# Optimization experiments

Hardware: AMD Instinct MI355X
Metric: run time of the kernel (lower is better)

Reference implementation:

```python
import jax, jax.numpy as jnp
import numpy as np
from jax import lax

SCORE_T = 0.05
NMS_T = 0.5
MAXDET = 300


def batch_iou(b1, b2):
    # b1: [K,4], b2: [K,4] -> [K,K]
    lt = jnp.maximum(b1[:, None, :2], b2[None, :, :2])
    rb = jnp.minimum(b1[:, None, 2:], b2[None, :, 2:])
    inter = jnp.clip(rb - lt, 0.0, None).prod(-1)
    a1 = (b1[:, 2:] - b1[:, :2]).prod(-1)
    a2 = (b2[:, 2:] - b2[:, :2]).prod(-1)
    union = a1[:, None] + a2[None, :] - inter
    return inter / jnp.clip(union, 1e-7, None)


def nms_class(boxes, cls_scores):
    # boxes: [N,4], cls_scores: [N]. Mirrors: score>thresh filter, top-k MAXDET
    # candidates, greedy NMS in descending score order.
    s = jnp.where(cls_scores > SCORE_T, cls_scores, -jnp.inf)
    top_s, idx = lax.top_k(s, MAXDET)          # sorted desc, [K]
    b = jnp.take(boxes, idx, axis=0)            # [K,4]
    v = jnp.isfinite(top_s)                     # passed score threshold
    iou = batch_iou(b, b)                       # [K,K]

    def body(kept, i):
        # keep i iff valid and no already-kept box has IoU >= NMS_T with it
        suppressed = jnp.any(jnp.where(kept, iou[i], 0.0) >= NMS_T)
        return kept.at[i].set(v[i] & ~suppressed), None

    kept, _ = lax.scan(body, jnp.zeros(MAXDET, dtype=bool), jnp.arange(MAXDET))
    return top_s, idx, kept


def per_image(boxes, cls):
    # boxes: [N,4], cls: [N,C]
    C = cls.shape[1]
    top_s, idx, kept = jax.vmap(nms_class, in_axes=(None, 1))(boxes, cls)  # [C,K]
    scores_flat = jnp.where(kept, top_s, -jnp.inf).reshape(-1)  # [C*K]
    idx_flat = idx.reshape(-1)
    labels_flat = jnp.repeat(jnp.arange(C), MAXDET)
    fs, fi = lax.top_k(scores_flat, MAXDET)     # global top-k across classes
    valid = jnp.isfinite(fs)
    box_idx = idx_flat[fi]
    out_boxes = jnp.where(valid[:, None], jnp.take(boxes, box_idx, axis=0), -1.0)
    out_scores = jnp.where(valid, fs, -1.0)
    out_labels = jnp.where(valid, labels_flat[fi], -1).astype(jnp.int32)
    return out_boxes, out_scores, out_labels


def setup_inputs() -> dict:
    key = jax.random.key(0)
    k1, k2, k3 = jax.random.split(key, 3)
    B, N, C = 8, 100000, 80
    centers = jax.random.uniform(k1, (B, N, 2), dtype=jnp.float32) * 1024.0
    wh = jax.random.uniform(k2, (B, N, 2), dtype=jnp.float32) * 96.0 + 4.0
    boxes = jnp.concatenate([centers - wh / 2, centers + wh / 2], axis=-1)
    classification = jax.random.uniform(k3, (B, N, C), dtype=jnp.float32)
    return {"boxes": boxes, "classification": classification}


def reference(boxes, classification):
    # Returns (Boxes [B,MAXDET,4], Scores [B,MAXDET], Labels [B,MAXDET] int32),
    # padded with -1 where fewer than MAXDET detections survive.
    return jax.vmap(per_image)(boxes, classification)
```

## Files before the change

kernel.cpp:

```cpp
#include <hip/hip_runtime.h>

#define BIMG 8
#define NBOX 100000
#define NCLS 80
#define KDET 300
#define CAP  2048
#define CAPC 12
#define TPUSH 0.9921875f
#define SCORE_T 0.05f
#define NELEM 8000000
#define NQ    2000000

typedef unsigned long long u64;
typedef unsigned u32;

#define OFF_PUSHCNT 0u
#define OFF_IMGDONE 2560u
#define ZERO_BYTES  2592u
#define OFF_BUF     4096u
#define OFF_KCNT    (4096u + 10485760u)
#define OFF_KSC     (OFF_KCNT + 2560u)
#define OFF_KIDX    (OFF_KSC + 768000u)

static __device__ __forceinline__ u64 mk_key(float sc, u32 n) {
  return ((u64)__float_as_uint(sc) << 32) | (u32)(~n);
}

static __device__ __forceinline__ void radix_step(const u32* hist, int nbins,
                                                  int width, u32* sk, u64* spfx,
                                                  u32* stot) {
  if (threadIdx.x < 64) {
    const int lane = threadIdx.x;
    const int chunk = nbins >> 6;
    u32 psum = 0;
    for (int i = 0; i < chunk; ++i) psum += hist[lane * chunk + i];
    u32 suf = psum;
#pragma unroll
    for (int off = 1; off < 64; off <<= 1) {
      u32 o = __shfl_down(suf, off);
      if (lane + off < 64) suf += o;
    }
    if (lane == 0) *stot = suf;
    u32 k = *sk;
    u64 bal = __ballot(suf >= k);
    if (bal != 0ull) {
      int L = 63 - __clzll((long long)bal);
      if (lane == L) {
        u32 krem = k - (suf - psum);
        int bi = (L + 1) * chunk - 1;
        u32 acc = 0;
        for (;;) {
          acc += hist[bi];
          if (acc >= krem || bi == L * chunk) break;
          --bi;
        }
        *spfx = (*spfx << width) | (u32)bi;
        *sk = krem - (acc - hist[bi]);
      }
    }
  }
}

__constant__ int RSH[6] = {53, 42, 31, 20, 9, 0};
__constant__ int RWD[6] = {11, 11, 11, 11, 11, 9};

static __device__ __forceinline__ void bitonic512(u64* tk, int t) {
  u64 a = tk[t];
#pragma unroll
  for (int k2 = 2; k2 <= 64; k2 <<= 1) {
#pragma unroll
    for (int j = k2 >> 1; j > 0; j >>= 1) {
      u64 c2 = __shfl_xor(a, j);
      bool takeMax = (((t & k2) == 0) == ((t & j) == 0));
      u64 mx = (a > c2) ? a : c2;
      u64 mn = (a > c2) ? c2 : a;
      a = takeMax ? mx : mn;
    }
  }
#pragma unroll
  for (int k2 = 128; k2 <= 512; k2 <<= 1) {
    for (int j = k2 >> 1; j >= 64; j >>= 1) {
      tk[t] = a;
      __syncthreads();
      u64 c2 = tk[t ^ j];
      bool takeMax = (((t & k2) == 0) == ((t & j) == 0));
      u64 mx = (a > c2) ? a : c2;
      u64 mn = (a > c2) ? c2 : a;
      a = takeMax ? mx : mn;
      __syncthreads();
    }
#pragma unroll
    for (int j = 32; j > 0; j >>= 1) {
      u64 c2 = __shfl_xor(a, j);
      bool takeMax = (((t & k2) == 0) == ((t & j) == 0));
      u64 mx = (a > c2) ? a : c2;
      u64 mn = (a > c2) ? c2 : a;
      a = takeMax ? mx : mn;
    }
  }
  tk[t] = a;
  __syncthreads();
}

static __device__ __forceinline__ void pushone(int c, float sc, u32 n, int b,
                                               u32* lcnt, u64* stage,
                                               u32* pushcnt, u64* buf) {
  u64 key = mk_key(sc, n);
  u32 slot = atomicAdd(&lcnt[c], 1u);
  if (slot < CAPC) {
    stage[c * CAPC + slot] = key;
  } else {
    u32 g = atomicAdd(&pushcnt[b * NCLS + c], 1u);
    if (g < CAP) buf[(size_t)(b * NCLS + c) * CAP + g] = key;
  }
}

__global__ __launch_bounds__(256) void histK(const float* __restrict__ cls,
                                             u32* __restrict__ pushcnt,
                                             u64* __restrict__ buf) {
  __shared__ u32 lcnt[NCLS];
  __shared__ u32 sbase[NCLS];
  __shared__ u64 stage[NCLS * CAPC];

  const int t = threadIdx.x;
  const int b = blockIdx.y;
  for (int i = t; i < NCLS; i += 256) lcnt[i] = 0;
  __syncthreads();

  const float4* base4 = (const float4*)(cls + (size_t)b * NELEM);
  const int start = blockIdx.x * 8192;

#define PROCQ(u) do { \
    float mx = fmaxf(fmaxf(v##u.x, v##u.y), fmaxf(v##u.z, v##u.w)); \
    if (mx >= TPUSH) { \
      const int e0 = q##u * 4; \
      const int c0 = e0 % NCLS; \
      const u32 n = (u32)(e0 / NCLS); \
      if (v##u.x >= TPUSH) pushone(c0 + 0, v##u.x, n, b, lcnt, stage, pushcnt, buf); \
      if (v##u.y >= TPUSH) pushone(c0 + 1, v##u.y, n, b, lcnt, stage, pushcnt, buf); \
      if (v##u.z >= TPUSH) pushone(c0 + 2, v##u.z, n, b, lcnt, stage, pushcnt, buf); \
      if (v##u.w >= TPUSH) pushone(c0 + 3, v##u.w, n, b, lcnt, stage, pushcnt, buf); \
    } } while (0)

  if (start + 8192 <= NQ) {
    for (int it = 0; it < 4; ++it) {
      const int qb = start + it * 2048 + t;
#define LOADF(u) const int q##u = qb + (u) * 256; const float4 v##u = base4[q##u]
      LOADF(0); LOADF(1); LOADF(2); LOADF(3);
      LOADF(4); LOADF(5); LOADF(6); LOADF(7);
#undef LOADF
      PROCQ(0); PROCQ(1); PROCQ(2); PROCQ(3);
      PROCQ(4); PROCQ(5); PROCQ(6); PROCQ(7);
    }
  } else {
    for (int it = 0; it < 4; ++it) {
      const int qb = start + it * 2048 + t;
#define LOADC(u) const int q##u = qb + (u) * 256; \
  const float4 v##u = (q##u < NQ) ? base4[q##u] : make_float4(0.f, 0.f, 0.f, 0.f)
      LOADC(0); LOADC(1); LOADC(2); LOADC(3);
      LOADC(4); LOADC(5); LOADC(6); LOADC(7);
#undef LOADC
      PROCQ(0); PROCQ(1); PROCQ(2); PROCQ(3);
      PROCQ(4); PROCQ(5); PROCQ(6); PROCQ(7);
    }
  }
#undef PROCQ
  __syncthreads();

  if (t < NCLS) {
    u32 cnt = min(lcnt[t], (u32)CAPC);
    sbase[t] = cnt ? atomicAdd(&pushcnt[b * NCLS + t], cnt) : 0u;
  }
  __syncthreads();
  for (int idx = t; idx < NCLS * CAPC; idx += 256) {
    const int c = idx / CAPC;
    const int k = idx - c * CAPC;
    if ((u32)k < min(lcnt[c], (u32)CAPC)) {
      u32 s = sbase[c] + (u32)k;
      if (s < CAP) buf[(size_t)(b * NCLS + c) * CAP + s] = stage[idx];
    }
  }
}

__global__ __launch_bounds__(512) void nmsK(const float* __restrict__ boxes,
                                            const float* __restrict__ cls,
                                            const u32* __restrict__ pushcnt,
                                            u64* __restrict__ buf,
                                            u32* __restrict__ keptCnt,
                                            float* __restrict__ keptScore,
                                            u32* __restrict__ keptIdx,
                                            u32* __restrict__ imgDone,
                                            float* __restrict__ out) {
  __shared__ float bx[KDET][4];
  __shared__ float scl[KDET];
  __shared__ u32 nn_[KDET];
  __shared__ u64 msk[KDET][5];
  __shared__ u64 tk[512];
  __shared__ u64 keptw[5];
  __shared__ u64 spfx;
  __shared__ u64 sand, sor;
  __shared__ u32 sk, stot, stcnt, smtot, smerge;
  __shared__ int msc[NCLS];
  __shared__ u32 sfpfx, sfk, sfab, sfeq, sfmode, sfbcnt;

  const int t = threadIdx.x;
  const int bc = blockIdx.x;
  const int b = bc / NCLS;
  u64* bufp = buf + (size_t)bc * CAP;
  u32* hist = (u32*)&msk[0][0];

  if (t == 0) { spfx = 0ull; sk = KDET; stcnt = 0u; sfmode = 0u; sfbcnt = 0u; }

  u32 realcnt = pushcnt[bc];
  const bool dofb = !(realcnt >= (u32)KDET && realcnt <= (u32)CAP);
  if (dofb) {
    const int c = bc % NCLS;
    const float* col = cls + (size_t)b * NELEM + c;
    for (int r = 0; r < 3; ++r) {
      const int shift = (r == 0) ? 21 : (r == 1) ? 10 : 0;
      const int nbins = (r == 2) ? 1024 : 2048;
      for (int i = t; i < nbins; i += 512) hist[i] = 0;
      __syncthreads();
      for (int n = t; n < NBOX; n += 512) {
        float sc = col[(size_t)n * NCLS];
        if (sc > SCORE_T) {
          u32 u = __float_as_uint(sc);
          bool ok = (r == 0) || (r == 1 ? ((u >> 21) == (sfpfx >> 21))
                                        : ((u >> 10) == (sfpfx >> 10)));
          if (ok) atomicAdd(&hist[(u >> shift) & (u32)(nbins - 1)], 1u);
        }
      }
      __syncthreads();
      if (t == 0) {
        if (r == 0) {
          u32 s = 0;
          for (int i = 0; i < nbins; ++i) s += hist[i];
          if (s < KDET) sfmode = 1u;
        }
        if (sfmode == 0u) {
          u32 kk2 = (r == 0) ? (u32)KDET : sfk;
          u32 acc = 0;
          int bi = nbins - 1;
          for (; bi >= 0; --bi) {
            if (acc + hist[bi] >= kk2) break;
            acc += hist[bi];
          }
          sfk = kk2 - acc;
          sfpfx = ((r == 0) ? 0u : sfpfx) | ((u32)bi << shift);
          if (r == 2) { sfeq = hist[bi]; sfab = KDET - sfk; }
        }
      }
      __syncthreads();
      if (sfmode == 1u) break;
    }

    if (sfmode == 1u) {
      for (int n = t; n < NBOX; n += 512) {
        float sc = col[(size_t)n * NCLS];
        if (sc > SCORE_T) {
          u32 g = atomicAdd(&sfbcnt, 1u);
          if (g < CAP) bufp[g] = mk_key(sc, (u32)n);
        }
      }
    } else {
      const u32 ustar = sfpfx;
      const u32 m = sfab, e = sfeq;
      if (m + e <= CAP) {
        for (int n = t; n < NBOX; n += 512) {
          float sc = col[(size_t)n * NCLS];
          if (sc > SCORE_T && __float_as_uint(sc) >= ustar) {
            u32 g = atomicAdd(&sfbcnt, 1u);
            if (g < CAP) bufp[g] = mk_key(sc, (u32)n);
          }
        }
      } else {
        for (int n = t; n < NBOX; n += 512) {
          float sc = col[(size_t)n * NCLS];
          if (sc > SCORE_T && __float_as_uint(sc) > ustar) {
            u32 g = atomicAdd(&sfbcnt, 1u);
            if (g < CAP) bufp[g] = mk_key(sc, (u32)n);
          }
        }
        __syncthreads();
        if (t == 0) {
          u32 room = CAP - m, got = 0;
          for (int n = 0; n < NBOX && got < room; ++n) {
            float sc = col[(size_t)n * NCLS];
            if (sc > SCORE_T && __float_as_uint(sc) == ustar) {
              u32 g = atomicAdd(&sfbcnt, 1u);
              if (g < CAP) bufp[g] = mk_key(sc, (u32)n);
              ++got;
            }
          }
        }
      }
    }
    __threadfence_block();
    __syncthreads();
    realcnt = sfbcnt;
  }
  const int cnt = min((int)realcnt, CAP);

  u64 kk[4];
#pragma unroll
  for (int u = 0; u < 4; ++u) {
    int i = t + u * 512;
    u64 v = 0ull;
    if (i < cnt)
      v = dofb ? *((volatile const u64*)(bufp + i)) : bufp[i];
    kk[u] = v;
  }

  const bool normal = (cnt > KDET);
  if (normal) {
    if (t == 0) { sand = ~0ull; sor = 0ull; }
    __syncthreads();
    {
      u64 ka = ~0ull, ko = 0ull;
#pragma unroll
      for (int u = 0; u < 4; ++u) {
        u64 key = kk[u];
        if (key) { ka &= key; ko |= key; }
      }
#pragma unroll
      for (int off = 32; off > 0; off >>= 1) {
        ka &= __shfl_xor(ka, off);
        ko |= __shfl_xor(ko, off);
      }
      if ((t & 63) == 0) {
        atomicAnd((unsigned long long*)&sand, (unsigned long long)ka);
        atomicOr((unsigned long long*)&sor, (unsigned long long)ko);
      }
    }
    __syncthreads();
    const u64 kand = sand, kor = sor;
    for (int p = 0; p < 6; ++p) {
      const int nb = (p == 5) ? 512 : 2048;
      const u32 mask = (u32)(nb - 1);
      const u32 ba = (u32)(kand >> RSH[p]) & mask;
      const u32 bo = (u32)(kor >> RSH[p]) & mask;
      if (ba == bo) {
        if (t == 0) spfx = (spfx << RWD[p]) | (u64)ba;
        __syncthreads();
        continue;
      }
      for (int i = t; i < nb; i += 512) hist[i] = 0;
      __syncthreads();
      const u64 pfx = spfx;
#pragma unroll
      for (int u = 0; u < 4; ++u) {
        u64 key = kk[u];
        if (!key) continue;
        if (p > 0 && (key >> RSH[p - 1]) != pfx) continue;
        atomicAdd(&hist[(u32)(key >> RSH[p]) & mask], 1u);
      }
      __syncthreads();
      radix_step(hist, nb, RWD[p], &sk, &spfx, &stot);
      __syncthreads();
    }
  } else {
    __syncthreads();
  }
  const u64 thr = normal ? spfx : 1ull;

  tk[t] = 0ull;
  __syncthreads();
#pragma unroll
  for (int u = 0; u < 4; ++u) {
    u64 key = kk[u];
    if (key >= thr && key != 0ull) {
      u32 pos = atomicAdd(&stcnt, 1u);
      if (pos < 512) tk[pos] = key;
    }
  }
  __syncthreads();

  bitonic512(tk, t);

  const int M = min((int)stcnt, KDET);
  for (int i = t; i < M; i += 512) {
    u64 key = tk[i];
    u32 n = ~(u32)key;
    scl[i] = __uint_as_float((u32)(key >> 32));
    nn_[i] = n;
    const float4 bv = *(const float4*)(boxes + ((size_t)b * NBOX + n) * 4);
    bx[i][0] = bv.x; bx[i][1] = bv.y; bx[i][2] = bv.z; bx[i][3] = bv.w;
  }
  __syncthreads();

  for (int i = t; i < M; i += 512) {
    float x1 = bx[i][0], y1 = bx[i][1], x2 = bx[i][2], y2 = bx[i][3];
    float a1 = (x2 - x1) * (y2 - y1);
    u64 m0 = 0, m1 = 0, m2 = 0, m3 = 0, m4 = 0;
    for (int j = 0; j < i; ++j) {
      float lx = fmaxf(x1, bx[j][0]);
      float ly = fmaxf(y1, bx[j][1]);
      float rx = fminf(x2, bx[j][2]);
      float ry = fminf(y2, bx[j][3]);
      float iw = fmaxf(rx - lx, 0.0f), ih = fmaxf(ry - ly, 0.0f);
      float inter = iw * ih;
      float a2 = (bx[j][2] - bx[j][0]) * (bx[j][3] - bx[j][1]);
      float uni = fmaxf(a1 + a2 - inter, 1e-7f);
      float iou = inter / uni;
      if (iou >= 0.5f) {
        u64 bit = 1ull << (j & 63);
        switch (j >> 6) {
          case 0: m0 |= bit; break;
          case 1: m1 |= bit; break;
          case 2: m2 |= bit; break;
          case 3: m3 |= bit; break;
          default: m4 |= bit; break;
        }
      }
    }
    msk[i][0] = m0; msk[i][1] = m1; msk[i][2] = m2; msk[i][3] = m3; msk[i][4] = m4;
  }
  __syncthreads();

  if (t < 64) {
    u64 kwv[5];
#pragma unroll
    for (int w = 0; w < 5; ++w) {
      const int i = w * 64 + t;
      bool pb = (i < M);
      u64 mown = 0ull;
      if (pb) {
#pragma unroll
        for (int w2 = 0; w2 < 5; ++w2)
          if (w2 < w && (msk[i][w2] & kwv[w2])) pb = false;
        mown = msk[i][w];
      }
      u64 kv = 0ull;
      for (;;) {
        u64 bal = __ballot(pb && ((mown & kv) == 0ull));
        if (!bal) break;
        int p = __ffsll((unsigned long long)bal) - 1;
        kv |= 1ull << p;
        if (t == p) pb = false;
      }
      kwv[w] = kv;
      if (t == 0) keptw[w] = kv;
    }
  }
  __syncthreads();

  for (int i = t; i < M; i += 512) {
    if ((keptw[i >> 6] >> (i & 63)) & 1ull) {
      int rank = 0;
      for (int w = 0; w < (i >> 6); ++w) rank += __popcll(keptw[w]);
      rank += __popcll(keptw[i >> 6] & ((1ull << (i & 63)) - 1ull));
      keptScore[(size_t)bc * KDET + rank] = scl[i];
      keptIdx[(size_t)bc * KDET + rank] = nn_[i];
    }
  }
  if (t == 0) {
    int tot = 0;
    for (int w = 0; w < 5; ++w) tot += __popcll(keptw[w]);
    keptCnt[bc] = (u32)tot;
  }
  __syncthreads();

  if (t == 0) {
    __threadfence();
    u32 done = atomicAdd(&imgDone[b], 1u);
    smerge = (done == NCLS - 1) ? 1u : 0u;
  }
  __syncthreads();
  if (!smerge) return;
  __threadfence();

  if (t == 0) { spfx = 0ull; sk = KDET; stcnt = 0u; smtot = 0u; sand = ~0ull; sor = 0ull; }
  if (t < NCLS) msc[t] = min((int)keptCnt[b * NCLS + t], KDET);
  __syncthreads();

  const float* ksc = keptScore + (size_t)b * NCLS * KDET;
#define MKEY(idx, key) do { \
    int c_ = (idx) / KDET, r_ = (idx) - c_ * KDET; \
    key = (r_ < msc[c_]) ? ((u64)__float_as_uint(ksc[idx]) << 32) | (u32)(~(u32)(idx)) \
                         : 0ull; \
  } while (0)

  {
    u64 ka = ~0ull, ko = 0ull;
    u32 mycnt = 0;
    for (int idx = t; idx < NCLS * KDET; idx += 512) {
      u64 key; MKEY(idx, key);
      if (key) { ka &= key; ko |= key; ++mycnt; }
    }
#pragma unroll
    for (int off = 32; off > 0; off >>= 1) {
      ka &= __shfl_xor(ka, off);
      ko |= __shfl_xor(ko, off);
      mycnt += __shfl_xor(mycnt, off);
    }
    if ((t & 63) == 0) {
      atomicAnd((unsigned long long*)&sand, (unsigned long long)ka);
      atomicOr((unsigned long long*)&sor, (unsigned long long)ko);
      atomicAdd(&smtot, mycnt);
    }
  }
  __syncthreads();

  const bool mnormal = ((int)smtot > KDET);
  if (mnormal) {
    const u64 kand = sand, kor = sor;
    for (int p = 0; p < 6; ++p) {
      const int nb = (p == 5) ? 512 : 2048;
      const u32 mask = (u32)(nb - 1);
      const u32 ba = (u32)(kand >> RSH[p]) & mask;
      const u32 bo = (u32)(kor >> RSH[p]) & mask;
      if (ba == bo) {
        if (t == 0) spfx = (spfx << RWD[p]) | (u64)ba;
        __syncthreads();
        continue;
      }
      for (int i = t; i < nb; i += 512) hist[i] = 0;
      __syncthreads();
      const u64 pfx = spfx;
      for (int idx = t; idx < NCLS * KDET; idx += 512) {
        u64 key; MKEY(idx, key);
        if (!key) continue;
        if (p > 0 && (key >> RSH[p - 1]) != pfx) continue;
        atomicAdd(&hist[(u32)(key >> RSH[p]) & mask], 1u);
      }
      __syncthreads();
      radix_step(hist, nb, RWD[p], &sk, &spfx, &stot);
      __syncthreads();
    }
  }
  const u64 mthr = mnormal ? spfx : 1ull;

  tk[t] = 0ull;
  __syncthreads();
  for (int idx = t; idx < NCLS * KDET; idx += 512) {
    u64 key; MKEY(idx, key);
    if (key >= mthr && key != 0ull) {
      u32 pos = atomicAdd(&stcnt, 1u);
      if (pos < 512) tk[pos] = key;
    }
  }
  __syncthreads();
#undef MKEY

  bitonic512(tk, t);

  if (t < KDET) {
    float* ob = out + ((size_t)b * KDET + t) * 4;
    float* os = out + (size_t)BIMG * KDET * 4;
    float* ol = os + (size_t)BIMG * KDET;
    u64 key = tk[t];
    if (key == 0ull) {
      *(float4*)ob = make_float4(-1.f, -1.f, -1.f, -1.f);
      os[(size_t)b * KDET + t] = -1.f;
      ol[(size_t)b * KDET + t] = -1.f;
    } else {
      u32 fi = ~(u32)key;
      int c = fi / KDET, r = fi - c * KDET;
      u32 n = keptIdx[((size_t)b * NCLS + c) * KDET + r];
      *(float4*)ob = *(const float4*)(boxes + ((size_t)b * NBOX + n) * 4);
      os[(size_t)b * KDET + t] = __uint_as_float((u32)(key >> 32));
      ol[(size_t)b * KDET + t] = (float)c;
    }
  }
}

extern "C" void kernel_launch(void* const* d_in, const int* in_sizes, int n_in,
                              void* d_out, int out_size, void* d_ws, size_t ws_size,
                              hipStream_t stream) {
  const float* boxes = (const float*)d_in[0];
  const float* cls = (const float*)d_in[1];
  float* out = (float*)d_out;
  char* ws = (char*)d_ws;

  u32* pushcnt = (u32*)(ws + OFF_PUSHCNT);
  u32* imgDone = (u32*)(ws + OFF_IMGDONE);
  u64* buf = (u64*)(ws + OFF_BUF);
  u32* keptCnt = (u32*)(ws + OFF_KCNT);
  float* keptScore = (float*)(ws + OFF_KSC);
  u32* keptIdx = (u32*)(ws + OFF_KIDX);

  (void)hipMemsetAsync(ws + OFF_PUSHCNT, 0, ZERO_BYTES, stream);

  histK<<<dim3(245, BIMG), 256, 0, stream>>>(cls, pushcnt, buf);
  nmsK<<<BIMG * NCLS, 512, 0, stream>>>(boxes, cls, pushcnt, buf, keptCnt,
                                        keptScore, keptIdx, imgDone, out);
}
```

Baseline: 543.9 us.

## Split merge into separate kernel, early-exit radix select, parallelize IoU mask rows

Moves the cross-class merge out of the last-finishing NMS block into its own kernel, which drops the imgDone atomic counter and the threadfence handshake. Both radix selections now stop early once the candidate set fits in 512 slots, saving histogram passes. Compaction uses wave ballots with a single atomic per wave instead of one atomic per element. The IoU mask is computed per (row, 64-column word) task, which evens out the triangular workload across threads. The cost is an extra kernel launch plus some added per-task setup.

```diff
diff --git a/kernel.cpp b/kernel.cpp
--- a/kernel.cpp
+++ b/kernel.cpp
@@ -15,8 +15,7 @@
 typedef unsigned u32;
 
 #define OFF_PUSHCNT 0u
-#define OFF_IMGDONE 2560u
-#define ZERO_BYTES  2592u
+#define ZERO_BYTES  2560u
 #define OFF_BUF     4096u
 #define OFF_KCNT    (4096u + 10485760u)
 #define OFF_KSC     (OFF_KCNT + 2560u)
@@ -28,7 +27,7 @@
 
 static __device__ __forceinline__ void radix_step(const u32* hist, int nbins,
                                                   int width, u32* sk, u64* spfx,
-                                                  u32* stot) {
+                                                  u32* ssel) {
   if (threadIdx.x < 64) {
     const int lane = threadIdx.x;
     const int chunk = nbins >> 6;
@@ -40,7 +39,6 @@
       u32 o = __shfl_down(suf, off);
       if (lane + off < 64) suf += o;
     }
-    if (lane == 0) *stot = suf;
     u32 k = *sk;
     u64 bal = __ballot(suf >= k);
     if (bal != 0ull) {
@@ -56,6 +54,7 @@
         }
         *spfx = (*spfx << width) | (u32)bi;
         *sk = krem - (acc - hist[bi]);
+        *ssel = (suf - psum) + acc;
       }
     }
   }
@@ -188,9 +187,7 @@
                                             u64* __restrict__ buf,
                                             u32* __restrict__ keptCnt,
                                             float* __restrict__ keptScore,
-                                            u32* __restrict__ keptIdx,
-                                            u32* __restrict__ imgDone,
-                                            float* __restrict__ out) {
+                                            u32* __restrict__ keptIdx) {
   __shared__ float bx[KDET][4];
   __shared__ float scl[KDET];
   __shared__ u32 nn_[KDET];
@@ -199,8 +196,7 @@
   __shared__ u64 keptw[5];
   __shared__ u64 spfx;
   __shared__ u64 sand, sor;
-  __shared__ u32 sk, stot, stcnt, smtot, smerge;
-  __shared__ int msc[NCLS];
+  __shared__ u32 sk, ssel, stcnt;
   __shared__ u32 sfpfx, sfk, sfab, sfeq, sfmode, sfbcnt;
 
   const int t = threadIdx.x;
@@ -312,6 +308,8 @@
   }
 
   const bool normal = (cnt > KDET);
+  int eshift = 0;
+  u64 ethr = 1ull;
   if (normal) {
     if (t == 0) { sand = ~0ull; sor = 0ull; }
     __syncthreads();
@@ -347,6 +345,7 @@
       for (int i = t; i < nb; i += 512) hist[i] = 0;
       __syncthreads();
       const u64 pfx = spfx;
+      const u32 skPrev = sk;
 #pragma unroll
       for (int u = 0; u < 4; ++u) {
         u64 key = kk[u];
@@ -355,22 +354,33 @@
         atomicAdd(&hist[(u32)(key >> RSH[p]) & mask], 1u);
       }
       __syncthreads();
-      radix_step(hist, nb, RWD[p], &sk, &spfx, &stot);
-      __syncthreads();
-    }
-  } else {
-    __syncthreads();
-  }
-  const u64 thr = normal ? spfx : 1ull;
+      radix_step(hist, nb, RWD[p], &sk, &spfx, &ssel);
+      __syncthreads();
+      if ((u32)KDET - skPrev + ssel <= 512u) { eshift = RSH[p]; break; }
+    }
+    ethr = spfx;
+  }
 
   tk[t] = 0ull;
   __syncthreads();
-#pragma unroll
-  for (int u = 0; u < 4; ++u) {
-    u64 key = kk[u];
-    if (key >= thr && key != 0ull) {
-      u32 pos = atomicAdd(&stcnt, 1u);
-      if (pos < 512) tk[pos] = key;
+  {
+    const int lane = t & 63;
+    const u64 lmlt = (1ull << lane) - 1ull;
+#pragma unroll
+    for (int u = 0; u < 4; ++u) {
+      u64 key = kk[u];
+      bool q = (key != 0ull) && ((key >> eshift) >= ethr);
+      u64 bal = __ballot(q);
+      u32 nw = (u32)__popcll(bal);
+      if (nw) {
+        u32 base = 0;
+        if (lane == 0) base = atomicAdd(&stcnt, nw);
+        base = __shfl(base, 0);
+        if (q) {
+          u32 pos = base + (u32)__popcll(bal & lmlt);
+          if (pos < 512) tk[pos] = key;
+        }
+      }
     }
   }
   __syncthreads();
@@ -388,32 +398,29 @@
   }
   __syncthreads();
 
-  for (int i = t; i < M; i += 512) {
-    float x1 = bx[i][0], y1 = bx[i][1], x2 = bx[i][2], y2 = bx[i][3];
-    float a1 = (x2 - x1) * (y2 - y1);
-    u64 m0 = 0, m1 = 0, m2 = 0, m3 = 0, m4 = 0;
-    for (int j = 0; j < i; ++j) {
-      float lx = fmaxf(x1, bx[j][0]);
-      float ly = fmaxf(y1, bx[j][1]);
-      float rx = fminf(x2, bx[j][2]);
-      float ry = fminf(y2, bx[j][3]);
-      float iw = fmaxf(rx - lx, 0.0f), ih = fmaxf(ry - ly, 0.0f);
-      float inter = iw * ih;
-      float a2 = (bx[j][2] - bx[j][0]) * (bx[j][3] - bx[j][1]);
-      float uni = fmaxf(a1 + a2 - inter, 1e-7f);
-      float iou = inter / uni;
-      if (iou >= 0.5f) {
-        u64 bit = 1ull << (j & 63);
-        switch (j >> 6) {
-          case 0: m0 |= bit; break;
-          case 1: m1 |= bit; break;
-          case 2: m2 |= bit; break;
-          case 3: m3 |= bit; break;
-          default: m4 |= bit; break;
-        }
-      }
-    }
-    msk[i][0] = m0; msk[i][1] = m1; msk[i][2] = m2; msk[i][3] = m3; msk[i][4] = m4;
+  for (int tau = t; tau < KDET * 5; tau += 512) {
+    const int i = tau / 5;
+    const int w = tau - i * 5;
+    u64 m = 0ull;
+    const int jb = w << 6;
+    if (i < M && jb < i) {
+      const int je = min(i, jb + 64);
+      const float x1 = bx[i][0], y1 = bx[i][1], x2 = bx[i][2], y2 = bx[i][3];
+      const float a1 = (x2 - x1) * (y2 - y1);
+      for (int j = jb; j < je; ++j) {
+        float lx = fmaxf(x1, bx[j][0]);
+        float ly = fmaxf(y1, bx[j][1]);
+        float rx = fminf(x2, bx[j][2]);
+        float ry = fminf(y2, bx[j][3]);
+        float iw = fmaxf(rx - lx, 0.0f), ih = fmaxf(ry - ly, 0.0f);
+        float inter = iw * ih;
+        float a2 = (bx[j][2] - bx[j][0]) * (bx[j][3] - bx[j][1]);
+        float uni = fmaxf(a1 + a2 - inter, 1e-7f);
+        float iou = inter / uni;
+        if (iou >= 0.5f) m |= 1ull << (j & 63);
+      }
+    }
+    if (i < M) msk[i][w] = m;
   }
   __syncthreads();
 
@@ -458,19 +465,25 @@
     for (int w = 0; w < 5; ++w) tot += __popcll(keptw[w]);
     keptCnt[bc] = (u32)tot;
   }
-  __syncthreads();
-
+}
+
+__global__ __launch_bounds__(512) void mergeK(const float* __restrict__ boxes,
+                                              const u32* __restrict__ keptCnt,
+                                              const float* __restrict__ keptScore,
+                                              const u32* __restrict__ keptIdx,
+                                              float* __restrict__ out) {
+  __shared__ u32 hist[2048];
+  __shared__ int msc[NCLS];
+  __shared__ u64 tk[512];
+  __shared__ u64 spfx, sand, sor;
+  __shared__ u32 sk, ssel, stcnt, smtot;
+
+  const int t = threadIdx.x;
+  const int b = blockIdx.x;
+  if (t < NCLS) msc[t] = min((int)keptCnt[b * NCLS + t], KDET);
   if (t == 0) {
-    __threadfence();
-    u32 done = atomicAdd(&imgDone[b], 1u);
-    smerge = (done == NCLS - 1) ? 1u : 0u;
-  }
-  __syncthreads();
-  if (!smerge) return;
-  __threadfence();
-
-  if (t == 0) { spfx = 0ull; sk = KDET; stcnt = 0u; smtot = 0u; sand = ~0ull; sor = 0ull; }
-  if (t < NCLS) msc[t] = min((int)keptCnt[b * NCLS + t], KDET);
+    spfx = 0ull; sk = KDET; stcnt = 0u; smtot = 0u; sand = ~0ull; sor = 0ull;
+  }
   __syncthreads();
 
   const float* ksc = keptScore + (size_t)b * NCLS * KDET;
@@ -502,6 +515,8 @@
   __syncthreads();
 
   const bool mnormal = ((int)smtot > KDET);
+  int eshift = 0;
+  u64 ethr = 1ull;
   if (mnormal) {
     const u64 kand = sand, kor = sor;
     for (int p = 0; p < 6; ++p) {
@@ -517,6 +532,7 @@
       for (int i = t; i < nb; i += 512) hist[i] = 0;
       __syncthreads();
       const u64 pfx = spfx;
+      const u32 skPrev = sk;
       for (int idx = t; idx < NCLS * KDET; idx += 512) {
         u64 key; MKEY(idx, key);
         if (!key) continue;
@@ -524,19 +540,34 @@
         atomicAdd(&hist[(u32)(key >> RSH[p]) & mask], 1u);
       }
       __syncthreads();
-      radix_step(hist, nb, RWD[p], &sk, &spfx, &stot);
-      __syncthreads();
-    }
-  }
-  const u64 mthr = mnormal ? spfx : 1ull;
+      radix_step(hist, nb, RWD[p], &sk, &spfx, &ssel);
+      __syncthreads();
+      if ((u32)KDET - skPrev + ssel <= 512u) { eshift = RSH[p]; break; }
+    }
+    ethr = spfx;
+  }
 
   tk[t] = 0ull;
   __syncthreads();
-  for (int idx = t; idx < NCLS * KDET; idx += 512) {
-    u64 key; MKEY(idx, key);
-    if (key >= mthr && key != 0ull) {
-      u32 pos = atomicAdd(&stcnt, 1u);
-      if (pos < 512) tk[pos] = key;
+  {
+    const int lane = t & 63;
+    const u64 lmlt = (1ull << lane) - 1ull;
+    for (int i0 = 0; i0 < NCLS * KDET; i0 += 512) {
+      const int idx = i0 + t;
+      u64 key = 0ull;
+      if (idx < NCLS * KDET) MKEY(idx, key);
+      bool q = (key != 0ull) && ((key >> eshift) >= ethr);
+      u64 bal = __ballot(q);
+      u32 nw = (u32)__popcll(bal);
+      if (nw) {
+        u32 base = 0;
+        if (lane == 0) base = atomicAdd(&stcnt, nw);
+        base = __shfl(base, 0);
+        if (q) {
+          u32 pos = base + (u32)__popcll(bal & lmlt);
+          if (pos < 512) tk[pos] = key;
+        }
+      }
     }
   }
   __syncthreads();
@@ -573,7 +604,6 @@
   char* ws = (char*)d_ws;
 
   u32* pushcnt = (u32*)(ws + OFF_PUSHCNT);
-  u32* imgDone = (u32*)(ws + OFF_IMGDONE);
   u64* buf = (u64*)(ws + OFF_BUF);
   u32* keptCnt = (u32*)(ws + OFF_KCNT);
   float* keptScore = (float*)(ws + OFF_KSC);
@@ -583,5 +613,6 @@
 
   histK<<<dim3(245, BIMG), 256, 0, stream>>>(cls, pushcnt, buf);
   nmsK<<<BIMG * NCLS, 512, 0, stream>>>(boxes, cls, pushcnt, buf, keptCnt,
-                                        keptScore, keptIdx, imgDone, out);
-}
+                                        keptScore, keptIdx);
+  mergeK<<<BIMG, 512, 0, stream>>>(boxes, keptCnt, keptScore, keptIdx, out);
+}
```

Result: faster. 523.0 us (-3.8%).
